# Kernel tuning notes

Measured on AMD Instinct MI355X. Metric: run time of the kernel, lower is better.

Reference implementation:

```python
import jax, jax.numpy as jnp
import numpy as np

NUM_HEADS = 16
LN_EPS = 1e-5


def setup_inputs() -> dict:
    key = jax.random.key(0)
    ks = jax.random.split(key, 6)
    B, N, D = 4, 4096, 1024
    s = 1.0 / np.sqrt(D)
    return {
        "x": jax.random.normal(ks[0], (B, N, D), dtype=jnp.float32),
        "Wq": jax.random.normal(ks[1], (D, D), dtype=jnp.float32) * s,
        "Wk": jax.random.normal(ks[2], (D, D), dtype=jnp.float32) * s,
        "Wv": jax.random.normal(ks[3], (D, D), dtype=jnp.float32) * s,
        "Wo": jax.random.normal(ks[4], (D, D), dtype=jnp.float32) * s,
        "bo": jnp.zeros((D,), dtype=jnp.float32),
        "alpha": jax.random.uniform(ks[5], (1,), dtype=jnp.float32),
        "temperature": jnp.float32(1.0),
        "gamma": jnp.ones((D,), dtype=jnp.float32),
        "beta": jnp.zeros((D,), dtype=jnp.float32),
    }


def _layernorm(x, gamma, beta):
    mu = jnp.mean(x, axis=-1, keepdims=True)
    var = jnp.var(x, axis=-1, keepdims=True)
    return (x - mu) * jax.lax.rsqrt(var + LN_EPS) * gamma + beta


def reference(x, Wq, Wk, Wv, Wo, bo, alpha, temperature, gamma, beta):
    B, N, D = x.shape
    H = NUM_HEADS
    hd = D // H
    residual = x
    # projections (query=None -> query comes from x), nn.Linear: x @ W.T
    q = (x @ Wq.T).reshape(B, N, H, hd).transpose(0, 2, 1, 3)  # [B,H,N,hd]
    k = (x @ Wk.T).reshape(B, N, H, hd).transpose(0, 2, 1, 3)
    v = (x @ Wv.T).reshape(B, N, H, hd).transpose(0, 2, 1, 3)
    # kk = K^T K + alpha*I, per (batch, head): [B,H,hd,hd]
    kk = jnp.einsum('bhnd,bhne->bhde', k, k)
    kk = kk + alpha[0] * jnp.eye(hd, dtype=x.dtype)
    kk_inv = jnp.linalg.inv(kk)
    # attn_map = kk_inv @ K^T @ V : [B,H,hd,hd]
    ktv = jnp.einsum('bhnd,bhne->bhde', k, v)
    attn_map = kk_inv @ ktv
    attn_map = jax.nn.softmax(attn_map / temperature, axis=-2)
    out = q @ attn_map  # [B,H,N,hd]
    out = out.transpose(0, 2, 1, 3).reshape(B, N, D)
    out = out @ Wo.T + bo
    return _layernorm(out + residual, gamma, beta)
```

## Files before the change

kernel.cpp:

```cpp
#include <hip/hip_runtime.h>
#include <cstdint>
#include <cstddef>

typedef unsigned short u16;
typedef __bf16 bf16x8 __attribute__((ext_vector_type(8)));
typedef float f32x4 __attribute__((ext_vector_type(4)));
typedef u16 u16x8 __attribute__((ext_vector_type(8)));
typedef u16 u16x4 __attribute__((ext_vector_type(4)));

#define NB 4
#define NN 4096
#define ND 1024
#define NH 16
#define NTOK (NB * NN)

__device__ __forceinline__ u16 f2bf(float f) {
    unsigned u = __float_as_uint(f);
    u += 0x7fffu + ((u >> 16) & 1u);
    return (u16)(u >> 16);
}

__device__ __forceinline__ void gload_lds16(const void* g, void* l) {
    __builtin_amdgcn_global_load_lds(
        (const __attribute__((address_space(1))) void*)g,
        (__attribute__((address_space(3))) void*)l, 16, 0, 0);
}

__global__ __launch_bounds__(256) void prep_cast(
    const float* __restrict__ x,
    const float* __restrict__ wq, const float* __restrict__ wk,
    const float* __restrict__ wv, const float* __restrict__ wo,
    u16* __restrict__ xb, u16* __restrict__ wb)
{
    const int n_x4 = (NTOK * ND) / 4;
    const int n_w4 = (ND * ND) / 4;
    const int total = n_x4 + 4 * n_w4;
    for (int i = blockIdx.x * blockDim.x + threadIdx.x; i < total;
         i += gridDim.x * blockDim.x) {
        float4 v;
        u16* dst;
        if (i < n_x4) {
            v = ((const float4*)x)[i];
            dst = xb + (size_t)i * 4;
        } else {
            int j = i - n_x4;
            int w = j / n_w4;
            int off = j - w * n_w4;
            const float* src = (w == 0) ? wq : (w == 1) ? wk : (w == 2) ? wv : wo;
            v = ((const float4*)src)[off];
            dst = wb + (size_t)j * 4;
        }
        u16x4 o;
        o[0] = f2bf(v.x); o[1] = f2bf(v.y); o[2] = f2bf(v.z); o[3] = f2bf(v.w);
        *(u16x4*)dst = o;
    }
}

template <int OUT_MODE>
__global__ __launch_bounds__(256, 2) void gemm_bt(
    const u16* __restrict__ A, int lda,
    const u16* __restrict__ Bw, int ldb,
    void* __restrict__ Cout, int ldc, int K,
    const float* __restrict__ bias, const float* __restrict__ resid,
    int rows_per_batch, size_t b_stride)
{
    __shared__ alignas(16) u16 lA[256 * 64];
    __shared__ alignas(16) u16 lB[128 * 64];

    const int tid = threadIdx.x;
    const int wv = tid >> 6, lane = tid & 63;
    const int quad = lane >> 4, lrow = lane & 15;

    const int orig = blockIdx.y * gridDim.x + blockIdx.x;
    const int cpx = (gridDim.x * gridDim.y) >> 3;
    const int wgid = (orig & 7) * cpx + (orig >> 3);
    const int bx = wgid % gridDim.x;
    const int by = wgid / gridDim.x;

    const int row0 = by * 256, col0 = bx * 128;
    const int wm = (wv >> 1) * 128, wn = (wv & 1) * 64;

    const u16* Bp = Bw + (b_stride ? (size_t)(row0 / rows_per_batch) * b_stride : 0);

    f32x4 acc[8][4] = {};

    const int srow = lane >> 3;
    const int cswE = ((lane & 7) ^ srow) * 8;

    for (int k0 = 0; k0 < K; k0 += 64) {
        __syncthreads();
#pragma unroll
        for (int i = 0; i < 8; ++i) {
            int rb = wv * 64 + i * 8;
            gload_lds16(A + (size_t)(row0 + rb + srow) * lda + k0 + cswE,
                        &lA[rb * 64]);
        }
#pragma unroll
        for (int i = 0; i < 4; ++i) {
            int rb = wv * 32 + i * 8;
            gload_lds16(Bp + (size_t)(col0 + rb + srow) * ldb + k0 + cswE,
                        &lB[rb * 64]);
        }
        __syncthreads();

#pragma unroll
        for (int kc = 0; kc < 2; ++kc) {
            const int ch = ((kc * 4 + quad) ^ (lrow & 7)) * 8;
            bf16x8 bfv[4];
#pragma unroll
            for (int t = 0; t < 4; ++t)
                bfv[t] = *(const bf16x8*)&lB[(wn + t * 16 + lrow) * 64 + ch];
#pragma unroll
            for (int mt = 0; mt < 8; ++mt) {
                bf16x8 af = *(const bf16x8*)&lA[(wm + mt * 16 + lrow) * 64 + ch];
#pragma unroll
                for (int nt = 0; nt < 4; ++nt)
                    acc[mt][nt] = __builtin_amdgcn_mfma_f32_16x16x32_bf16(
                        af, bfv[nt], acc[mt][nt], 0, 0, 0);
            }
        }
    }

    float bvals[4];
    if (OUT_MODE == 1) {
#pragma unroll
        for (int nt = 0; nt < 4; ++nt)
            bvals[nt] = bias[col0 + wn + nt * 16 + lrow];
    }
#pragma unroll
    for (int mt = 0; mt < 8; ++mt)
#pragma unroll
        for (int nt = 0; nt < 4; ++nt)
#pragma unroll
            for (int r = 0; r < 4; ++r) {
                int grow = row0 + wm + mt * 16 + quad * 4 + r;
                int gcol = col0 + wn + nt * 16 + lrow;
                if (OUT_MODE == 0) {
                    ((u16*)Cout)[(size_t)grow * ldc + gcol] = f2bf(acc[mt][nt][r]);
                } else {
                    float vv = acc[mt][nt][r] + bvals[nt] +
                               resid[(size_t)grow * ldc + gcol];
                    ((float*)Cout)[(size_t)grow * ldc + gcol] = vv;
                }
            }
}

__global__ __launch_bounds__(256) void stage2a_kernel(
    const u16* __restrict__ qkv,
    float* __restrict__ Part)
{
    __shared__ alignas(16) u16 sKt[4][64][40];
    __shared__ alignas(16) u16 sVt[4][64][40];
    __shared__ float S[64][132];

    const int tid = threadIdx.x;
    const int wv = tid >> 6, lane = tid & 63;
    const int quad = lane >> 4, lrow = lane & 15;
    const int bh = blockIdx.x, split = blockIdx.y;
    const int b = bh >> 4, h = bh & 15;

    f32x4 akk[4][4] = {};
    f32x4 aktv[4][4] = {};
    const u16* kbase = qkv + ND + h * 64;
    const u16* vbase = qkv + 2 * ND + h * 64;
    const size_t tok0 = (size_t)b * NN;

    for (int it = 0; it < 2; ++it) {
        const int n0 = split * 256 + wv * 64 + it * 32;
#pragma unroll
        for (int pass = 0; pass < 4; ++pass) {
            int nl = pass * 8 + (lane >> 3);
            int d0 = (lane & 7) * 8;
            size_t roff = (tok0 + n0 + nl) * 3072 + d0;
            u16x8 kvv = *(const u16x8*)(kbase + roff);
            u16x8 vvv = *(const u16x8*)(vbase + roff);
#pragma unroll
            for (int j = 0; j < 8; ++j) {
                sKt[wv][d0 + j][nl] = kvv[j];
                sVt[wv][d0 + j][nl] = vvv[j];
            }
        }
        bf16x8 fK[4], fV[4];
#pragma unroll
        for (int t = 0; t < 4; ++t) {
            fK[t] = *(const bf16x8*)&sKt[wv][t * 16 + lrow][quad * 8];
            fV[t] = *(const bf16x8*)&sVt[wv][t * 16 + lrow][quad * 8];
        }
#pragma unroll
        for (int mt = 0; mt < 4; ++mt)
#pragma unroll
            for (int et = 0; et < 4; ++et) {
                akk[mt][et] = __builtin_amdgcn_mfma_f32_16x16x32_bf16(
                    fK[mt], fK[et], akk[mt][et], 0, 0, 0);
                aktv[mt][et] = __builtin_amdgcn_mfma_f32_16x16x32_bf16(
                    fK[mt], fV[et], aktv[mt][et], 0, 0, 0);
            }
    }

    for (int w = 0; w < 4; ++w) {
        if (wv == w) {
#pragma unroll
            for (int mt = 0; mt < 4; ++mt)
#pragma unroll
                for (int et = 0; et < 4; ++et)
#pragma unroll
                    for (int r = 0; r < 4; ++r) {
                        int row = mt * 16 + quad * 4 + r;
                        int col = et * 16 + lrow;
                        if (w == 0) {
                            S[row][col] = akk[mt][et][r];
                            S[row][64 + col] = aktv[mt][et][r];
                        } else {
                            S[row][col] += akk[mt][et][r];
                            S[row][64 + col] += aktv[mt][et][r];
                        }
                    }
        }
        __syncthreads();
    }

    float* dst = Part + (size_t)(bh * 16 + split) * 8192;
#pragma unroll
    for (int c = 0; c < 8; ++c) {
        int idx = tid * 4 + c * 1024;
        int row = idx >> 7, col = idx & 127;
        float4 v = *(const float4*)&S[row][col];
        ((float4*)dst)[idx >> 2] = v;
    }
}

__global__ __launch_bounds__(256) void stage2b_kernel(
    const float* __restrict__ Part,
    const u16* __restrict__ wb,
    const float* __restrict__ alpha,
    const float* __restrict__ temp,
    u16* __restrict__ Mout)
{
    __shared__ float S[64][132];
    __shared__ float colbuf[2][64];
    __shared__ alignas(16) u16 sAttn[64][72];

    const int tid = threadIdx.x;
    const int wv = tid >> 6, lane = tid & 63;
    const int quad = lane >> 4, lrow = lane & 15;
    const int b = blockIdx.x >> 4, h = blockIdx.x & 15;

    const float* Pb = Part + (size_t)blockIdx.x * 16 * 8192;
#pragma unroll
    for (int c = 0; c < 8; ++c) {
        int idx = tid * 4 + c * 1024;
        float4 a = ((const float4*)Pb)[idx >> 2];
#pragma unroll
        for (int s = 1; s < 16; ++s) {
            float4 t4 = ((const float4*)(Pb + (size_t)s * 8192))[idx >> 2];
            a.x += t4.x; a.y += t4.y; a.z += t4.z; a.w += t4.w;
        }
        int row = idx >> 7, col = idx & 127;
        *(float4*)&S[row][col] = a;
    }
    __syncthreads();

    const float aval = alpha[0];
    const int c0 = wv * 32;
    float R[32];
#pragma unroll
    for (int j = 0; j < 32; ++j) {
        R[j] = S[lane][c0 + j];
        if (c0 + j == lane) R[j] += aval;
    }
    if (wv == 0) colbuf[0][lane] = R[0];
    __syncthreads();

    float mydiag = 1.0f;
    for (int p = 0; p < 64; ++p) {
        const int cur = p & 1;
        float cv = colbuf[cur][lane];
        float pv = colbuf[cur][p];
        if (p == lane) mydiag = pv;
        float m = (lane == p) ? 0.0f : cv * __builtin_amdgcn_rcpf(pv);
#pragma unroll
        for (int j = 0; j < 32; ++j) {
            float rowv = __uint_as_float(
                __builtin_amdgcn_readlane(__float_as_uint(R[j]), p));
            R[j] -= m * rowv;
        }
        if (p < 63) {
            int pn = p + 1;
            if (wv == (pn >> 5)) colbuf[cur ^ 1][lane] = R[pn & 31];
        }
        __syncthreads();
    }

    if (wv >= 2) {
        const float idg = __builtin_amdgcn_rcpf(mydiag) * (1.0f / temp[0]);
#pragma unroll
        for (int j = 0; j < 32; ++j) {
            float xv = R[j] * idg;
            float mx = xv;
#pragma unroll
            for (int off = 32; off > 0; off >>= 1)
                mx = fmaxf(mx, __shfl_xor(mx, off, 64));
            float ev = __expf(xv - mx);
            float sum = ev;
#pragma unroll
            for (int off = 32; off > 0; off >>= 1)
                sum += __shfl_xor(sum, off, 64);
            sAttn[lane][(wv - 2) * 32 + j] = f2bf(ev * __builtin_amdgcn_rcpf(sum));
        }
    }
    __syncthreads();

    {
        bf16x8 fB[4][2];
#pragma unroll
        for (int nt = 0; nt < 4; ++nt)
#pragma unroll
            for (int ks = 0; ks < 2; ++ks)
                fB[nt][ks] = *(const bf16x8*)&sAttn[nt * 16 + lrow][ks * 32 + quad * 8];

        const u16* wo = wb + (size_t)3072 * ND + h * 64;
        u16* Mb = Mout + (size_t)b * ND * ND + h * 64;
        for (int i = 0; i < 16; ++i) {
            int mt = wv * 16 + i;
            int oA = mt * 16 + lrow;
            bf16x8 fA[2];
#pragma unroll
            for (int ks = 0; ks < 2; ++ks)
                fA[ks] = *(const bf16x8*)(wo + (size_t)oA * ND + ks * 32 + quad * 8);
#pragma unroll
            for (int nt = 0; nt < 4; ++nt) {
                f32x4 acc = {};
                acc = __builtin_amdgcn_mfma_f32_16x16x32_bf16(fA[0], fB[nt][0], acc, 0, 0, 0);
                acc = __builtin_amdgcn_mfma_f32_16x16x32_bf16(fA[1], fB[nt][1], acc, 0, 0, 0);
#pragma unroll
                for (int r = 0; r < 4; ++r) {
                    int o = mt * 16 + quad * 4 + r;
                    Mb[(size_t)o * ND + nt * 16 + lrow] = f2bf(acc[r]);
                }
            }
        }
    }
}

__global__ __launch_bounds__(256) void ln_kernel(
    const float* __restrict__ y, const float* __restrict__ gamma,
    const float* __restrict__ beta, float* __restrict__ out)
{
    const int row = blockIdx.x, tid = threadIdx.x;
    const float4 v = ((const float4*)(y + (size_t)row * ND))[tid];
    float s = v.x + v.y + v.z + v.w;
    float q = v.x * v.x + v.y * v.y + v.z * v.z + v.w * v.w;
#pragma unroll
    for (int off = 32; off > 0; off >>= 1) {
        s += __shfl_xor(s, off, 64);
        q += __shfl_xor(q, off, 64);
    }
    __shared__ float ss[4], sq[4];
    const int wv = tid >> 6;
    if ((tid & 63) == 0) { ss[wv] = s; sq[wv] = q; }
    __syncthreads();
    s = ss[0] + ss[1] + ss[2] + ss[3];
    q = sq[0] + sq[1] + sq[2] + sq[3];
    const float mu = s * (1.0f / ND);
    const float var = q * (1.0f / ND) - mu * mu;
    const float rs = rsqrtf(var + 1e-5f);
    const float4 g = ((const float4*)gamma)[tid];
    const float4 bt = ((const float4*)beta)[tid];
    float4 o;
    o.x = (v.x - mu) * rs * g.x + bt.x;
    o.y = (v.y - mu) * rs * g.y + bt.y;
    o.z = (v.z - mu) * rs * g.z + bt.z;
    o.w = (v.w - mu) * rs * g.w + bt.w;
    ((float4*)(out + (size_t)row * ND))[tid] = o;
}

extern "C" void kernel_launch(void* const* d_in, const int* in_sizes, int n_in,
                              void* d_out, int out_size, void* d_ws, size_t ws_size,
                              hipStream_t stream)
{
    const float* x     = (const float*)d_in[0];
    const float* Wq    = (const float*)d_in[1];
    const float* Wk    = (const float*)d_in[2];
    const float* Wv    = (const float*)d_in[3];
    const float* Wo    = (const float*)d_in[4];
    const float* bo    = (const float*)d_in[5];
    const float* alpha = (const float*)d_in[6];
    const float* temp  = (const float*)d_in[7];
    const float* gamma = (const float*)d_in[8];
    const float* beta  = (const float*)d_in[9];

    char* ws = (char*)d_ws;
    u16* xb   = (u16*)(ws);
    float* Part = (float*)(ws);
    u16* wb   = (u16*)(ws + 33554432);
    u16* qkv  = (u16*)(ws + 41943040);
    u16* Mb   = (u16*)(ws + 142606336);
    float* y  = (float*)(ws + 150994944);
    float* out = (float*)d_out;

    prep_cast<<<dim3(4096), dim3(256), 0, stream>>>(x, Wq, Wk, Wv, Wo, xb, wb);

    gemm_bt<0><<<dim3(24, 64), dim3(256), 0, stream>>>(
        xb, 1024, wb, 1024, (void*)qkv, 3072, 1024,
        nullptr, nullptr, 1 << 30, (size_t)0);

    stage2a_kernel<<<dim3(64, 16), dim3(256), 0, stream>>>(qkv, Part);
    stage2b_kernel<<<dim3(64), dim3(256), 0, stream>>>(Part, wb, alpha, temp, Mb);

    gemm_bt<1><<<dim3(8, 64), dim3(256), 0, stream>>>(
        qkv, 3072, Mb, 1024, (void*)y, 1024, 1024,
        bo, x, 4096, (size_t)(1024 * 1024));

    ln_kernel<<<dim3(16384), dim3(256), 0, stream>>>(y, gamma, beta, out);
}
```

Before: 394.1 us.

## Restructure GEMM into 256x256 tiles with 4-stage async LDS pipeline

Rewrites the bf16 GEMM to use 512-thread blocks computing 256x256 output tiles. The K loop now runs in 32-wide chunks with a 4-deep ring of LDS buffers filled by global_load_lds, so loads for later chunks are in flight while MFMAs run on the current one. Explicit vmcnt waits and raw barriers replace the old sync pairs, and s_setprio raises priority around the MFMA block. The cost is fewer workgroups, 128KB of LDS per block, and a new swizzled layout whose indexing has to be exactly right.

```diff
diff --git a/kernel.cpp b/kernel.cpp
--- a/kernel.cpp
+++ b/kernel.cpp
@@ -57,15 +57,14 @@
 }
 
 template <int OUT_MODE>
-__global__ __launch_bounds__(256, 2) void gemm_bt(
+__global__ __launch_bounds__(512, 2) void gemm_bt(
     const u16* __restrict__ A, int lda,
     const u16* __restrict__ Bw, int ldb,
     void* __restrict__ Cout, int ldc, int K,
     const float* __restrict__ bias, const float* __restrict__ resid,
     int rows_per_batch, size_t b_stride)
 {
-    __shared__ alignas(16) u16 lA[256 * 64];
-    __shared__ alignas(16) u16 lB[128 * 64];
+    __shared__ alignas(16) u16 lds[4][2][128 * 64];
 
     const int tid = threadIdx.x;
     const int wv = tid >> 6, lane = tid & 63;
@@ -77,68 +76,92 @@
     const int bx = wgid % gridDim.x;
     const int by = wgid / gridDim.x;
 
-    const int row0 = by * 256, col0 = bx * 128;
-    const int wm = (wv >> 1) * 128, wn = (wv & 1) * 64;
+    const int row0 = by * 256, col0 = bx * 256;
+    const int wm = wv >> 2, wn = wv & 3;
 
     const u16* Bp = Bw + (b_stride ? (size_t)(row0 / rows_per_batch) * b_stride : 0);
 
+    const int clog = (lane & 7) ^ (lane >> 3);
+    const int srcR = 2 * (lane >> 3) + (clog >> 2);
+    const int srcK = (clog & 3) * 8;
+
+    const int choff = ((((lrow & 1) * 4) + quad) ^ (lrow >> 1)) * 8;
+    const int aoff = (wm * 64 + (lrow >> 1)) * 64 + choff;
+    const int boff = (wn * 32 + (lrow >> 1)) * 64 + choff;
+
     f32x4 acc[8][4] = {};
 
-    const int srow = lane >> 3;
-    const int cswE = ((lane & 7) ^ srow) * 8;
-
-    for (int k0 = 0; k0 < K; k0 += 64) {
-        __syncthreads();
-#pragma unroll
-        for (int i = 0; i < 8; ++i) {
-            int rb = wv * 64 + i * 8;
-            gload_lds16(A + (size_t)(row0 + rb + srow) * lda + k0 + cswE,
-                        &lA[rb * 64]);
-        }
-#pragma unroll
-        for (int i = 0; i < 4; ++i) {
-            int rb = wv * 32 + i * 8;
-            gload_lds16(Bp + (size_t)(col0 + rb + srow) * ldb + k0 + cswE,
-                        &lB[rb * 64]);
-        }
-        __syncthreads();
-
-#pragma unroll
-        for (int kc = 0; kc < 2; ++kc) {
-            const int ch = ((kc * 4 + quad) ^ (lrow & 7)) * 8;
-            bf16x8 bfv[4];
-#pragma unroll
-            for (int t = 0; t < 4; ++t)
-                bfv[t] = *(const bf16x8*)&lB[(wn + t * 16 + lrow) * 64 + ch];
-#pragma unroll
-            for (int mt = 0; mt < 8; ++mt) {
-                bf16x8 af = *(const bf16x8*)&lA[(wm + mt * 16 + lrow) * 64 + ch];
-#pragma unroll
-                for (int nt = 0; nt < 4; ++nt)
-                    acc[mt][nt] = __builtin_amdgcn_mfma_f32_16x16x32_bf16(
-                        af, bfv[nt], acc[mt][nt], 0, 0, 0);
-            }
-        }
+    auto stage = [&](int c) {
+        const int kbase = c * 32;
+        u16* uA = &lds[c & 3][0][0];
+        u16* uB = &lds[c & 3][1][0];
+#pragma unroll
+        for (int i = 0; i < 2; ++i) {
+            const int r0 = wv * 32 + i * 16;
+            const int ldst = (wv * 16 + i * 8) * 64;
+            gload_lds16(A + (size_t)(row0 + r0 + srcR) * lda + kbase + srcK,
+                        uA + ldst);
+            gload_lds16(Bp + (size_t)(col0 + r0 + srcR) * ldb + kbase + srcK,
+                        uB + ldst);
+        }
+    };
+
+    auto compute = [&](int c) {
+        const u16* uA = &lds[c & 3][0][0];
+        const u16* uB = &lds[c & 3][1][0];
+        bf16x8 bfv[4];
+#pragma unroll
+        for (int n = 0; n < 4; ++n)
+            bfv[n] = *(const bf16x8*)&uB[boff + n * 512];
+        __builtin_amdgcn_s_setprio(1);
+#pragma unroll
+        for (int m = 0; m < 8; ++m) {
+            bf16x8 af = *(const bf16x8*)&uA[aoff + m * 512];
+#pragma unroll
+            for (int n = 0; n < 4; ++n)
+                acc[m][n] = __builtin_amdgcn_mfma_f32_16x16x32_bf16(
+                    af, bfv[n], acc[m][n], 0, 0, 0);
+        }
+        __builtin_amdgcn_s_setprio(0);
+    };
+
+    const int NC = K >> 5;
+
+    stage(0); stage(1); stage(2);
+
+#pragma unroll 1
+    for (int c = 0; c < NC; ++c) {
+        if (c + 3 < NC) stage(c + 3);
+        if (c + 3 < NC)      asm volatile("s_waitcnt vmcnt(12)" ::: "memory");
+        else if (c + 2 < NC) asm volatile("s_waitcnt vmcnt(8)"  ::: "memory");
+        else if (c + 1 < NC) asm volatile("s_waitcnt vmcnt(4)"  ::: "memory");
+        else                 asm volatile("s_waitcnt vmcnt(0)"  ::: "memory");
+        __builtin_amdgcn_s_barrier();
+        asm volatile("" ::: "memory");
+        compute(c);
+        asm volatile("" ::: "memory");
+        __builtin_amdgcn_s_barrier();
+        asm volatile("" ::: "memory");
     }
 
     float bvals[4];
     if (OUT_MODE == 1) {
 #pragma unroll
-        for (int nt = 0; nt < 4; ++nt)
-            bvals[nt] = bias[col0 + wn + nt * 16 + lrow];
+        for (int nt2 = 0; nt2 < 4; ++nt2)
+            bvals[nt2] = bias[col0 + wn * 64 + nt2 * 16 + lrow];
     }
 #pragma unroll
     for (int mt = 0; mt < 8; ++mt)
 #pragma unroll
-        for (int nt = 0; nt < 4; ++nt)
+        for (int nt2 = 0; nt2 < 4; ++nt2)
 #pragma unroll
             for (int r = 0; r < 4; ++r) {
-                int grow = row0 + wm + mt * 16 + quad * 4 + r;
-                int gcol = col0 + wn + nt * 16 + lrow;
+                int grow = row0 + wm * 128 + mt * 16 + quad * 4 + r;
+                int gcol = col0 + wn * 64 + nt2 * 16 + lrow;
                 if (OUT_MODE == 0) {
-                    ((u16*)Cout)[(size_t)grow * ldc + gcol] = f2bf(acc[mt][nt][r]);
+                    ((u16*)Cout)[(size_t)grow * ldc + gcol] = f2bf(acc[mt][nt2][r]);
                 } else {
-                    float vv = acc[mt][nt][r] + bvals[nt] +
+                    float vv = acc[mt][nt2][r] + bvals[nt2] +
                                resid[(size_t)grow * ldc + gcol];
                     ((float*)Cout)[(size_t)grow * ldc + gcol] = vv;
                 }
@@ -400,14 +423,14 @@
 
     prep_cast<<<dim3(4096), dim3(256), 0, stream>>>(x, Wq, Wk, Wv, Wo, xb, wb);
 
-    gemm_bt<0><<<dim3(24, 64), dim3(256), 0, stream>>>(
+    gemm_bt<0><<<dim3(12, 64), dim3(512), 0, stream>>>(
         xb, 1024, wb, 1024, (void*)qkv, 3072, 1024,
         nullptr, nullptr, 1 << 30, (size_t)0);
 
     stage2a_kernel<<<dim3(64, 16), dim3(256), 0, stream>>>(qkv, Part);
     stage2b_kernel<<<dim3(64), dim3(256), 0, stream>>>(Part, wb, alpha, temp, Mb);
 
-    gemm_bt<1><<<dim3(8, 64), dim3(256), 0, stream>>>(
+    gemm_bt<1><<<dim3(4, 64), dim3(512), 0, stream>>>(
         qkv, 3072, Mb, 1024, (void*)y, 1024, 1024,
         bo, x, 4096, (size_t)(1024 * 1024));
 
```

Result: slower. 412.3 us (+4.6%).

## Fuse output GEMM with residual add and LayerNorm; halve stage2a split count

Applied to the files above, without the earlier changes.

Replaces the second GEMM and the separate LayerNorm kernel with one kernel. Each block computes a 32-row strip across all 1024 columns, adds bias and residual, reduces row statistics in registers and LDS, and writes the normalized output directly. This removes the fp32 intermediate y round trip and one launch. In exchange it uses only 512 blocks with small M tiles, a large accumulator array, and no double buffering, which may lower MFMA efficiency. Separately, stage2a now uses 8 splits instead of 16, so stage2b has fewer partial sums to reduce.

```diff
diff --git a/kernel.cpp b/kernel.cpp
--- a/kernel.cpp
+++ b/kernel.cpp
@@ -145,6 +145,137 @@
             }
 }
 
+__global__ __launch_bounds__(256, 3) void gemm2_ln(
+    const u16* __restrict__ A,
+    const u16* __restrict__ Mball,
+    const float* __restrict__ bias,
+    const float* __restrict__ resid,
+    const float* __restrict__ gamma,
+    const float* __restrict__ beta,
+    float* __restrict__ out)
+{
+    __shared__ alignas(16) u16 lA[32 * 64];
+    __shared__ alignas(16) u16 lB[256 * 64];
+    __shared__ float red[4][32][2];
+
+    const int tid = threadIdx.x;
+    const int wv = tid >> 6, lane = tid & 63;
+    const int quad = lane >> 4, lrow = lane & 15;
+
+    const int orig = blockIdx.x;
+    const int wgid = (orig & 7) * 64 + (orig >> 3);
+    const int row0 = wgid * 32;
+    const u16* Bp = Mball + (size_t)(row0 >> 12) * ND * ND;
+
+    const int srow = lane >> 3;
+    const int cswE = ((lane & 7) ^ srow) * 8;
+
+    f32x4 acc[4][2][4] = {};
+
+#pragma unroll
+    for (int nc = 0; nc < 4; ++nc) {
+        const int ncol0 = nc * 256;
+#pragma unroll 1
+        for (int k0 = 0; k0 < 1024; k0 += 64) {
+            __syncthreads();
+            gload_lds16(A + (size_t)(row0 + wv * 8 + srow) * 3072 + k0 + cswE,
+                        &lA[(wv * 8) * 64]);
+#pragma unroll
+            for (int i = 0; i < 8; ++i) {
+                int rb = wv * 64 + i * 8;
+                gload_lds16(Bp + (size_t)(ncol0 + rb + srow) * ND + k0 + cswE,
+                            &lB[rb * 64]);
+            }
+            __syncthreads();
+#pragma unroll
+            for (int kc = 0; kc < 2; ++kc) {
+                const int ch = ((kc * 4 + quad) ^ (lrow & 7)) * 8;
+                bf16x8 bfv[4];
+#pragma unroll
+                for (int nt = 0; nt < 4; ++nt)
+                    bfv[nt] = *(const bf16x8*)&lB[(wv * 64 + nt * 16 + lrow) * 64 + ch];
+#pragma unroll
+                for (int mt = 0; mt < 2; ++mt) {
+                    bf16x8 af = *(const bf16x8*)&lA[(mt * 16 + lrow) * 64 + ch];
+#pragma unroll
+                    for (int nt = 0; nt < 4; ++nt)
+                        acc[nc][mt][nt] = __builtin_amdgcn_mfma_f32_16x16x32_bf16(
+                            af, bfv[nt], acc[nc][mt][nt], 0, 0, 0);
+                }
+            }
+        }
+    }
+
+    float s8[2][4] = {{0.f, 0.f, 0.f, 0.f}, {0.f, 0.f, 0.f, 0.f}};
+    float q8[2][4] = {{0.f, 0.f, 0.f, 0.f}, {0.f, 0.f, 0.f, 0.f}};
+#pragma unroll
+    for (int nc = 0; nc < 4; ++nc)
+#pragma unroll
+        for (int mt = 0; mt < 2; ++mt)
+#pragma unroll
+            for (int nt = 0; nt < 4; ++nt) {
+                const int gcol = nc * 256 + wv * 64 + nt * 16 + lrow;
+                const float bv = bias[gcol];
+#pragma unroll
+                for (int rr = 0; rr < 4; ++rr) {
+                    const int grow = row0 + mt * 16 + quad * 4 + rr;
+                    float v = acc[nc][mt][nt][rr] + bv +
+                              resid[(size_t)grow * ND + gcol];
+                    acc[nc][mt][nt][rr] = v;
+                    s8[mt][rr] += v;
+                    q8[mt][rr] += v * v;
+                }
+            }
+#pragma unroll
+    for (int mt = 0; mt < 2; ++mt)
+#pragma unroll
+        for (int rr = 0; rr < 4; ++rr)
+#pragma unroll
+            for (int off = 1; off <= 8; off <<= 1) {
+                s8[mt][rr] += __shfl_xor(s8[mt][rr], off, 64);
+                q8[mt][rr] += __shfl_xor(q8[mt][rr], off, 64);
+            }
+    if (lrow == 0) {
+#pragma unroll
+        for (int mt = 0; mt < 2; ++mt)
+#pragma unroll
+            for (int rr = 0; rr < 4; ++rr) {
+                const int rl = mt * 16 + quad * 4 + rr;
+                red[wv][rl][0] = s8[mt][rr];
+                red[wv][rl][1] = q8[mt][rr];
+            }
+    }
+    __syncthreads();
+    float mu8[2][4], rs8[2][4];
+#pragma unroll
+    for (int mt = 0; mt < 2; ++mt)
+#pragma unroll
+        for (int rr = 0; rr < 4; ++rr) {
+            const int rl = mt * 16 + quad * 4 + rr;
+            const float s = red[0][rl][0] + red[1][rl][0] + red[2][rl][0] + red[3][rl][0];
+            const float q = red[0][rl][1] + red[1][rl][1] + red[2][rl][1] + red[3][rl][1];
+            const float mu = s * (1.0f / ND);
+            const float var = q * (1.0f / ND) - mu * mu;
+            mu8[mt][rr] = mu;
+            rs8[mt][rr] = rsqrtf(var + 1e-5f);
+        }
+#pragma unroll
+    for (int nc = 0; nc < 4; ++nc)
+#pragma unroll
+        for (int mt = 0; mt < 2; ++mt)
+#pragma unroll
+            for (int nt = 0; nt < 4; ++nt) {
+                const int gcol = nc * 256 + wv * 64 + nt * 16 + lrow;
+                const float g = gamma[gcol], bt = beta[gcol];
+#pragma unroll
+                for (int rr = 0; rr < 4; ++rr) {
+                    const int grow = row0 + mt * 16 + quad * 4 + rr;
+                    out[(size_t)grow * ND + gcol] =
+                        (acc[nc][mt][nt][rr] - mu8[mt][rr]) * rs8[mt][rr] * g + bt;
+                }
+            }
+}
+
 __global__ __launch_bounds__(256) void stage2a_kernel(
     const u16* __restrict__ qkv,
     float* __restrict__ Part)
@@ -165,8 +296,8 @@
     const u16* vbase = qkv + 2 * ND + h * 64;
     const size_t tok0 = (size_t)b * NN;
 
-    for (int it = 0; it < 2; ++it) {
-        const int n0 = split * 256 + wv * 64 + it * 32;
+    for (int it = 0; it < 4; ++it) {
+        const int n0 = split * 512 + wv * 128 + it * 32;
 #pragma unroll
         for (int pass = 0; pass < 4; ++pass) {
             int nl = pass * 8 + (lane >> 3);
@@ -219,7 +350,7 @@
         __syncthreads();
     }
 
-    float* dst = Part + (size_t)(bh * 16 + split) * 8192;
+    float* dst = Part + (size_t)(bh * 8 + split) * 8192;
 #pragma unroll
     for (int c = 0; c < 8; ++c) {
         int idx = tid * 4 + c * 1024;
@@ -245,13 +376,13 @@
     const int quad = lane >> 4, lrow = lane & 15;
     const int b = blockIdx.x >> 4, h = blockIdx.x & 15;
 
-    const float* Pb = Part + (size_t)blockIdx.x * 16 * 8192;
+    const float* Pb = Part + (size_t)blockIdx.x * 8 * 8192;
 #pragma unroll
     for (int c = 0; c < 8; ++c) {
         int idx = tid * 4 + c * 1024;
         float4 a = ((const float4*)Pb)[idx >> 2];
 #pragma unroll
-        for (int s = 1; s < 16; ++s) {
+        for (int s = 1; s < 8; ++s) {
             float4 t4 = ((const float4*)(Pb + (size_t)s * 8192))[idx >> 2];
             a.x += t4.x; a.y += t4.y; a.z += t4.z; a.w += t4.w;
         }
@@ -340,38 +471,6 @@
             }
         }
     }
-}
-
-__global__ __launch_bounds__(256) void ln_kernel(
-    const float* __restrict__ y, const float* __restrict__ gamma,
-    const float* __restrict__ beta, float* __restrict__ out)
-{
-    const int row = blockIdx.x, tid = threadIdx.x;
-    const float4 v = ((const float4*)(y + (size_t)row * ND))[tid];
-    float s = v.x + v.y + v.z + v.w;
-    float q = v.x * v.x + v.y * v.y + v.z * v.z + v.w * v.w;
-#pragma unroll
-    for (int off = 32; off > 0; off >>= 1) {
-        s += __shfl_xor(s, off, 64);
-        q += __shfl_xor(q, off, 64);
-    }
-    __shared__ float ss[4], sq[4];
-    const int wv = tid >> 6;
-    if ((tid & 63) == 0) { ss[wv] = s; sq[wv] = q; }
-    __syncthreads();
-    s = ss[0] + ss[1] + ss[2] + ss[3];
-    q = sq[0] + sq[1] + sq[2] + sq[3];
-    const float mu = s * (1.0f / ND);
-    const float var = q * (1.0f / ND) - mu * mu;
-    const float rs = rsqrtf(var + 1e-5f);
-    const float4 g = ((const float4*)gamma)[tid];
-    const float4 bt = ((const float4*)beta)[tid];
-    float4 o;
-    o.x = (v.x - mu) * rs * g.x + bt.x;
-    o.y = (v.y - mu) * rs * g.y + bt.y;
-    o.z = (v.z - mu) * rs * g.z + bt.z;
-    o.w = (v.w - mu) * rs * g.w + bt.w;
-    ((float4*)(out + (size_t)row * ND))[tid] = o;
 }
 
 extern "C" void kernel_launch(void* const* d_in, const int* in_sizes, int n_in,
@@ -395,7 +494,6 @@
     u16* wb   = (u16*)(ws + 33554432);
     u16* qkv  = (u16*)(ws + 41943040);
     u16* Mb   = (u16*)(ws + 142606336);
-    float* y  = (float*)(ws + 150994944);
     float* out = (float*)d_out;
 
     prep_cast<<<dim3(4096), dim3(256), 0, stream>>>(x, Wq, Wk, Wv, Wo, xb, wb);
@@ -404,12 +502,9 @@
         xb, 1024, wb, 1024, (void*)qkv, 3072, 1024,
         nullptr, nullptr, 1 << 30, (size_t)0);
 
-    stage2a_kernel<<<dim3(64, 16), dim3(256), 0, stream>>>(qkv, Part);
+    stage2a_kernel<<<dim3(64, 8), dim3(256), 0, stream>>>(qkv, Part);
     stage2b_kernel<<<dim3(64), dim3(256), 0, stream>>>(Part, wb, alpha, temp, Mb);
 
-    gemm_bt<1><<<dim3(8, 64), dim3(256), 0, stream>>>(
-        qkv, 3072, Mb, 1024, (void*)y, 1024, 1024,
-        bo, x, 4096, (size_t)(1024 * 1024));
-
-    ln_kernel<<<dim3(16384), dim3(256), 0, stream>>>(y, gamma, beta, out);
-}
+    gemm2_ln<<<dim3(512), dim3(256), 0, stream>>>(
+        qkv, Mb, bo, x, gamma, beta, out);
+}
```

New measurement: 428.9 us. +8.8%, slower.
